# Kernel optimization log

Measured on AMD Instinct MI355X. Metric: run time of the kernel, lower is better.

## Reference

```python
import jax, jax.numpy as jnp
import numpy as np

N, E, D, H = 20000, 320000, 128, 256
NUM_FINE = 2


def _mlp(x, W1, b1, W2, b2):
    # Linear -> relu -> Linear -> relu (dropout rate 0.0 is identity)
    h = jax.nn.relu(x @ W1 + b1)
    return jax.nn.relu(h @ W2 + b2)


def setup_inputs() -> dict:
    key = jax.random.key(0)
    ks = jax.random.split(key, 12)

    def p(k, shape):
        fan_in = shape[0]
        return jax.random.normal(k, shape, jnp.float32) * (1.0 / fan_in) ** 0.5

    return {
        "nodes": jax.random.normal(ks[0], (N, D), jnp.float32),
        "edges": jax.random.normal(ks[1], (E, D), jnp.float32),
        "senders": jax.random.randint(ks[2], (E,), 0, N, jnp.int32),
        "receivers": jax.random.randint(ks[3], (E,), 0, N, jnp.int32),
        # embed node MLP: D -> H -> D
        "Wn1": p(ks[4], (D, H)), "bn1": jnp.zeros((H,), jnp.float32),
        "Wn2": p(ks[5], (H, D)), "bn2": jnp.zeros((D,), jnp.float32),
        # embed edge MLP: D -> H -> D
        "We1": p(ks[6], (D, H)), "be1": jnp.zeros((H,), jnp.float32),
        "We2": p(ks[7], (H, D)), "be2": jnp.zeros((D,), jnp.float32),
        # edge model MLP: 3D -> H -> D  (concat[src, dest, edge_attr])
        "Wed1": p(ks[8], (3 * D, H)), "bed1": jnp.zeros((H,), jnp.float32),
        "Wed2": p(ks[9], (H, D)), "bed2": jnp.zeros((D,), jnp.float32),
        # node model MLP: 2D -> H -> D  (concat[x, segment_sum(edge_attr)])
        "Wnd1": p(ks[10], (2 * D, H)), "bnd1": jnp.zeros((H,), jnp.float32),
        "Wnd2": p(ks[11], (H, D)), "bnd2": jnp.zeros((D,), jnp.float32),
    }


def reference(nodes, edges, senders, receivers,
              Wn1, bn1, Wn2, bn2, We1, be1, We2, be2,
              Wed1, bed1, Wed2, bed2, Wnd1, bnd1, Wnd2, bnd2):
    # Embed stage (EmbedMetaLayer)
    x = _mlp(nodes, Wn1, bn1, Wn2, bn2)   # (N, D)
    e = _mlp(edges, We1, be1, We2, be2)   # (E, D)

    pooled = []
    for _ in range(NUM_FINE):
        # EdgeModel: gather src/dest node feats, concat with edge feats, MLP
        edge_in = jnp.concatenate([x[senders], x[receivers], e], axis=-1)  # (E, 3D)
        e = _mlp(edge_in, Wed1, bed1, Wed2, bed2)                           # (E, D)
        # NodeModel: scatter-add edge feats to receiver nodes, concat, MLP
        agg = jax.ops.segment_sum(e, receivers, num_segments=N)            # (N, D)
        x = _mlp(jnp.concatenate([x, agg], axis=-1), Wnd1, bnd1, Wnd2, bnd2)  # (N, D)
        # global_add_pooling: vmap(jnp.sum) over nodes -> per-node feature sum (N,)
        pooled.append(jnp.sum(x, axis=-1))
    # concatenate along last axis of the 1-D pooled vectors -> (NUM_FINE * N,)
    return jnp.concatenate(pooled, axis=-1)
```

## Files before the change

kernel.cpp:

```cpp
#include <hip/hip_runtime.h>
#include <stdint.h>

#define N_NODES 20000
#define N_EDGES 320000

typedef __attribute__((ext_vector_type(8)))  __bf16        bf16x8;
typedef __attribute__((ext_vector_type(16))) float         f32x16;
typedef __attribute__((ext_vector_type(4)))  float         f32x4v;
typedef __attribute__((ext_vector_type(4)))  uint32_t      u32x4;
typedef __attribute__((ext_vector_type(8)))  unsigned short us8;
typedef __attribute__((ext_vector_type(2)))  unsigned short us2;

static __device__ __forceinline__ unsigned short cvt_bf16(float f) {
  uint32_t u = __builtin_bit_cast(uint32_t, f);
  u = (u + 0x7fffu + ((u >> 16) & 1u)) >> 16;
  return (unsigned short)u;
}
static __device__ __forceinline__ float cvt_f32(unsigned short h) {
  uint32_t u = ((uint32_t)h) << 16;
  return __builtin_bit_cast(float, u);
}

static __device__ __forceinline__ void gll16(const void* g, void* l) {
  __builtin_amdgcn_global_load_lds(
      (const __attribute__((address_space(1))) unsigned int*)g,
      (__attribute__((address_space(3))) unsigned int*)l, 16, 0, 0);
}

#define WAITV(n) do { \
  if ((n) == 0)      asm volatile("s_waitcnt vmcnt(0)" ::: "memory"); \
  else if ((n) == 2) asm volatile("s_waitcnt vmcnt(2)" ::: "memory"); \
  else if ((n) == 4) asm volatile("s_waitcnt vmcnt(4)" ::: "memory"); \
  else if ((n) == 6) asm volatile("s_waitcnt vmcnt(6)" ::: "memory"); \
  else               asm volatile("s_waitcnt vmcnt(8)" ::: "memory"); \
} while (0)

__global__ void pack_w(const float* __restrict__ W, unsigned short* __restrict__ out,
                       int K, int Ncols) {
  int idx = blockIdx.x * 256 + threadIdx.x;
  int total = K * Ncols;
  if (idx >= total) return;
  int e    = idx & 7;
  int lane = (idx >> 3) & 63;
  int t    = idx >> 9;
  int ntiles = Ncols >> 5;
  int nt = t % ntiles;
  int ks = t / ntiles;
  int k = ks * 16 + (lane >> 5) * 8 + e;
  int c = nt * 32 + (lane & 31);
  out[idx] = cvt_bf16(W[(size_t)k * Ncols + c]);
}

__global__ void pack_w2(const float* __restrict__ W, unsigned short* __restrict__ out) {
  int idx = blockIdx.x * 256 + threadIdx.x;
  if (idx >= 32768) return;
  int e    = idx & 7;
  int lane = (idx >> 3) & 63;
  int t    = idx >> 9;
  int nt = t & 3, ks = t >> 2;
  int k = ks * 16 + ((lane >> 5) << 2) + (e & 3) + ((e >> 2) << 3);
  int c = nt * 32 + (lane & 31);
  out[idx] = cvt_bf16(W[(size_t)k * 128 + c]);
}

__global__ void hist_k(const int* __restrict__ recv, int* __restrict__ cnt, int n) {
  int i = blockIdx.x * 256 + threadIdx.x;
  if (i < n) atomicAdd(&cnt[recv[i]], 1);
}

__global__ void scan_k(const int* __restrict__ cnt, int* __restrict__ off,
                       int* __restrict__ cursor, int n) {
  __shared__ int part[1024];
  int t = threadIdx.x;
  int chunk = (n + 1023) / 1024;
  int base = t * chunk;
  int s = 0;
  for (int i = 0; i < chunk; ++i) { int idx = base + i; if (idx < n) s += cnt[idx]; }
  part[t] = s;
  __syncthreads();
  for (int d = 1; d < 1024; d <<= 1) {
    int v = (t >= d) ? part[t - d] : 0;
    __syncthreads();
    part[t] += v;
    __syncthreads();
  }
  int prefix = (t > 0) ? part[t - 1] : 0;
  for (int i = 0; i < chunk; ++i) {
    int idx = base + i;
    if (idx < n) { off[idx] = prefix; cursor[idx] = prefix; prefix += cnt[idx]; }
  }
  if (t == 1023) off[n] = part[1023];
}

__global__ void fill_k(const int* __restrict__ recv, int* __restrict__ cursor,
                       int* __restrict__ eid, int n) {
  int i = blockIdx.x * 256 + threadIdx.x;
  if (i < n) {
    int p = atomicAdd(&cursor[recv[i]], 1);
    eid[p] = i;
  }
}

__global__ void agg_k(const unsigned short* __restrict__ eb, const int* __restrict__ off,
                      const int* __restrict__ eid, unsigned short* __restrict__ aggb, int n) {
  int node = blockIdx.x * 4 + (threadIdx.x >> 6);
  if (node >= n) return;
  int lane = threadIdx.x & 63;
  float a0 = 0.f, a1 = 0.f;
  int s = off[node], t = off[node + 1];
  for (int q = s; q < t; ++q) {
    int ei = eid[q];
    us2 v = *(const us2*)(eb + (size_t)ei * 128 + lane * 2);
    a0 += cvt_f32(v[0]);
    a1 += cvt_f32(v[1]);
  }
  us2 r; r[0] = cvt_bf16(a0); r[1] = cvt_bf16(a1);
  *(us2*)(aggb + (size_t)node * 128 + lane * 2) = r;
}

template <int KIN, int MODE, int POOL>
__global__ __launch_bounds__(256, 2)
void mlp_kernel(const float* __restrict__ srcf,
                const unsigned short* __restrict__ xb,
                const unsigned short* __restrict__ ebuf,
                const unsigned short* __restrict__ aggb,
                const int* __restrict__ senders,
                const int* __restrict__ receivers,
                const unsigned short* __restrict__ P1,
                const float* __restrict__ b1,
                const unsigned short* __restrict__ P2,
                const float* __restrict__ b2,
                unsigned short* __restrict__ dst,
                float* __restrict__ pool_out,
                int nrows) {
  constexpr int NS1 = KIN / 32;
  constexpr int ROWOPS = (MODE == 0) ? 4 : 2;
  __shared__ __align__(16) unsigned char lds[49152];

  const int tid  = threadIdx.x;
  const int lane = tid & 63;
  const int wid  = tid >> 6;
  const int g    = lane >> 5;
  const int l31  = lane & 31;
  const int rowBlock = blockIdx.x << 7;

  const unsigned char* P1b = (const unsigned char*)P1;
  const unsigned char* P2b = (const unsigned char*)P2;

  int grow = rowBlock + wid * 32 + l31;
  if (grow >= nrows) grow = nrows - 1;

  const unsigned short *pS = nullptr, *pR = nullptr, *pE = nullptr;
  const unsigned short *pX = nullptr, *pAg = nullptr;
  const float* fb = nullptr;
  if constexpr (MODE == 0) {
    fb = srcf + (size_t)grow * KIN;
  } else if constexpr (MODE == 1) {
    pS = xb + (size_t)senders[grow] * 128;
    pR = xb + (size_t)receivers[grow] * 128;
    pE = ebuf + (size_t)grow * 128;
  } else {
    pX  = xb + (size_t)grow * 128;
    pAg = aggb + (size_t)grow * 128;
  }

  auto STG1 = [&](int s) {
    unsigned char* bW = lds + (s % 3) * 16384;
#pragma unroll
    for (int c = 0; c < 4; ++c)
      gll16(P1b + (size_t)s * 16384 + c * 4096 + tid * 16,
            bW + c * 4096 + wid * 1024);
  };
  auto STG2 = [&](int c) {
    unsigned char* bW = lds + ((c + NS1) % 3) * 16384;
#pragma unroll
    for (int q = 0; q < 4; ++q)
      gll16(P2b + (size_t)c * 16384 + q * 4096 + tid * 16,
            bW + q * 4096 + wid * 1024);
  };

  auto LROW = [&](int s, us8* o) {
    const int k0s = s * 32;
    const unsigned short* p;
    if constexpr (MODE == 1) {
      const int seg = k0s >> 7;
      p = (seg == 0) ? pS : (seg == 1) ? pR : pE;
    } else {
      p = (k0s >> 7) ? pAg : pX;
    }
    const int ko = k0s & 127;
    o[0] = *(const us8*)(p + ko + g * 8);
    o[1] = *(const us8*)(p + ko + 16 + g * 8);
  };
  auto LROWF = [&](int s, f32x4v* rf) {
    const float* p = fb + s * 32 + g * 8;
    rf[0] = *(const f32x4v*)(p);
    rf[1] = *(const f32x4v*)(p + 4);
    rf[2] = *(const f32x4v*)(p + 16);
    rf[3] = *(const f32x4v*)(p + 20);
  };
  auto MKBR = [&](const f32x4v* rf, bf16x8& b0v, bf16x8& b1v) {
    us8 h0, h1;
#pragma unroll
    for (int e = 0; e < 4; ++e) {
      h0[e] = cvt_bf16(rf[0][e]); h0[4 + e] = cvt_bf16(rf[1][e]);
      h1[e] = cvt_bf16(rf[2][e]); h1[4 + e] = cvt_bf16(rf[3][e]);
    }
    b0v = __builtin_bit_cast(bf16x8, h0);
    b1v = __builtin_bit_cast(bf16x8, h1);
  };

  f32x16 acc1[8];
#pragma unroll
  for (int t = 0; t < 8; ++t)
#pragma unroll
    for (int k = 0; k < 16; ++k) acc1[t][k] = 0.0f;

  auto COMPUTE = [&](const unsigned char* bW, bf16x8 b0v, bf16x8 b1v) {
    __builtin_amdgcn_s_setprio(1);
#pragma unroll
    for (int kc = 0; kc < 2; ++kc) {
      const bf16x8 bv = kc ? b1v : b0v;
#pragma unroll
      for (int nt = 0; nt < 8; ++nt) {
        bf16x8 av = __builtin_bit_cast(bf16x8,
            *(const us8*)(bW + (kc * 8 + nt) * 1024 + lane * 16));
        acc1[nt] = __builtin_amdgcn_mfma_f32_32x32x16_bf16(av, bv, acc1[nt], 0, 0, 0);
      }
    }
    __builtin_amdgcn_s_setprio(0);
  };

  us8    rr[4][2];
  f32x4v rf[4][4];

  STG1(0);
  if constexpr (MODE == 0) { LROWF(0, rf[0]); LROWF(1, rf[1]); LROWF(2, rf[2]); }
  else                     { LROW(0, rr[0]);  LROW(1, rr[1]);  LROW(2, rr[2]); }

#pragma unroll
  for (int s = 0; s < NS1; ++s) {
    const int w = (s == 0) ? ROWOPS * 2 : ((s + 2 < NS1) ? ROWOPS : 0);
    WAITV(w);
    asm volatile("s_waitcnt lgkmcnt(0)" ::: "memory");
    asm volatile("s_barrier" ::: "memory");
    if (s + 1 < NS1) STG1(s + 1);
    if (s + 3 < NS1) {
      if constexpr (MODE == 0) LROWF(s + 3, rf[(s + 3) & 3]);
      else                     LROW(s + 3, rr[(s + 3) & 3]);
    }
    bf16x8 b0v, b1v;
    if constexpr (MODE == 0) MKBR(rf[s & 3], b0v, b1v);
    else { b0v = __builtin_bit_cast(bf16x8, rr[s & 3][0]);
           b1v = __builtin_bit_cast(bf16x8, rr[s & 3][1]); }
    COMPUTE(lds + (s % 3) * 16384, b0v, b1v);
  }

  STG2(0);
  STG2(1);

  u32x4 pa4[16];
#pragma unroll
  for (int t = 0; t < 8; ++t) {
#pragma unroll
    for (int q4 = 0; q4 < 4; ++q4) {
      const f32x4v bv4 = *(const f32x4v*)(b1 + t * 32 + q4 * 8 + g * 4);
      float v0 = fmaxf(acc1[t][q4 * 4 + 0] + bv4[0], 0.0f);
      float v1 = fmaxf(acc1[t][q4 * 4 + 1] + bv4[1], 0.0f);
      float v2 = fmaxf(acc1[t][q4 * 4 + 2] + bv4[2], 0.0f);
      float v3 = fmaxf(acc1[t][q4 * 4 + 3] + bv4[3], 0.0f);
      uint32_t lo, hi;
      asm("v_cvt_pk_bf16_f32 %0, %1, %2" : "=v"(lo) : "v"(v0), "v"(v1));
      asm("v_cvt_pk_bf16_f32 %0, %1, %2" : "=v"(hi) : "v"(v2), "v"(v3));
      pa4[t * 2 + (q4 >> 1)][(q4 & 1) * 2 + 0] = lo;
      pa4[t * 2 + (q4 >> 1)][(q4 & 1) * 2 + 1] = hi;
    }
  }

  f32x16 acc2[4];
#pragma unroll
  for (int nt = 0; nt < 4; ++nt)
#pragma unroll
    for (int k = 0; k < 16; ++k) acc2[nt][k] = 0.0f;

#pragma unroll
  for (int c = 0; c < 4; ++c) {
    WAITV(c < 3 ? 4 : 0);
    asm volatile("s_waitcnt lgkmcnt(0)" ::: "memory");
    asm volatile("s_barrier" ::: "memory");
    if (c + 2 < 4) STG2(c + 2);
    const unsigned char* bW = lds + ((c + NS1) % 3) * 16384;
    __builtin_amdgcn_s_setprio(1);
#pragma unroll
    for (int kk = 0; kk < 4; ++kk) {
      const bf16x8 a2 = __builtin_bit_cast(bf16x8, pa4[c * 4 + kk]);
#pragma unroll
      for (int nt = 0; nt < 4; ++nt) {
        const bf16x8 bw = __builtin_bit_cast(bf16x8,
            *(const us8*)(bW + (kk * 4 + nt) * 1024 + lane * 16));
        acc2[nt] = __builtin_amdgcn_mfma_f32_32x32x16_bf16(a2, bw, acc2[nt], 0, 0, 0);
      }
    }
    __builtin_amdgcn_s_setprio(0);
  }

  float bias2[4];
#pragma unroll
  for (int nt = 0; nt < 4; ++nt) bias2[nt] = b2[nt * 32 + l31];

#pragma unroll
  for (int reg = 0; reg < 16; ++reg) {
    const int rowpat = (reg & 3) + ((reg >> 2) << 3) + g * 4;
    const int row = rowBlock + wid * 32 + rowpat;
    float vs = 0.0f;
#pragma unroll
    for (int nt = 0; nt < 4; ++nt) {
      float v = fmaxf(acc2[nt][reg] + bias2[nt], 0.0f);
      vs += v;
      if (row < nrows) dst[(size_t)row * 128 + nt * 32 + l31] = cvt_bf16(v);
    }
    if constexpr (POOL) {
#pragma unroll
      for (int m = 1; m <= 16; m <<= 1) vs += __shfl_xor(vs, m, 64);
      if (l31 == 0 && row < nrows) pool_out[row] = vs;
    }
  }
}

static constexpr size_t OFF_X    = 0;
static constexpr size_t OFF_E    = 5120000;
static constexpr size_t OFF_AGG  = 87040000;
static constexpr size_t OFF_PN1  = 92160000;
static constexpr size_t OFF_PN2  = OFF_PN1 + 65536;
static constexpr size_t OFF_PE1  = OFF_PN2 + 65536;
static constexpr size_t OFF_PE2  = OFF_PE1 + 65536;
static constexpr size_t OFF_PD1  = OFF_PE2 + 65536;
static constexpr size_t OFF_PD2  = OFF_PD1 + 196608;
static constexpr size_t OFF_PM1  = OFF_PD2 + 65536;
static constexpr size_t OFF_PM2  = OFF_PM1 + 131072;
static constexpr size_t OFF_CNT  = OFF_PM2 + 65536;
static constexpr size_t OFF_OFFS = OFF_CNT + 80000;
static constexpr size_t OFF_CUR  = OFF_OFFS + 80004;
static constexpr size_t OFF_EID  = OFF_CUR + 80000;

extern "C" void kernel_launch(void* const* d_in, const int* in_sizes, int n_in,
                              void* d_out, int out_size, void* d_ws, size_t ws_size,
                              hipStream_t stream) {
  const float* nodes = (const float*)d_in[0];
  const float* edges = (const float*)d_in[1];
  const int* senders = (const int*)d_in[2];
  const int* receivers = (const int*)d_in[3];
  const float* Wn1 = (const float*)d_in[4];  const float* bn1 = (const float*)d_in[5];
  const float* Wn2 = (const float*)d_in[6];  const float* bn2 = (const float*)d_in[7];
  const float* We1 = (const float*)d_in[8];  const float* be1 = (const float*)d_in[9];
  const float* We2 = (const float*)d_in[10]; const float* be2 = (const float*)d_in[11];
  const float* Wed1 = (const float*)d_in[12]; const float* bed1 = (const float*)d_in[13];
  const float* Wed2 = (const float*)d_in[14]; const float* bed2 = (const float*)d_in[15];
  const float* Wnd1 = (const float*)d_in[16]; const float* bnd1 = (const float*)d_in[17];
  const float* Wnd2 = (const float*)d_in[18]; const float* bnd2 = (const float*)d_in[19];

  char* ws = (char*)d_ws;
  unsigned short* xb   = (unsigned short*)(ws + OFF_X);
  unsigned short* eb   = (unsigned short*)(ws + OFF_E);
  unsigned short* aggb = (unsigned short*)(ws + OFF_AGG);
  unsigned short* Pn1  = (unsigned short*)(ws + OFF_PN1);
  unsigned short* Pn2  = (unsigned short*)(ws + OFF_PN2);
  unsigned short* Pe1  = (unsigned short*)(ws + OFF_PE1);
  unsigned short* Pe2  = (unsigned short*)(ws + OFF_PE2);
  unsigned short* Pd1  = (unsigned short*)(ws + OFF_PD1);
  unsigned short* Pd2  = (unsigned short*)(ws + OFF_PD2);
  unsigned short* Pm1  = (unsigned short*)(ws + OFF_PM1);
  unsigned short* Pm2  = (unsigned short*)(ws + OFF_PM2);
  int* cnt    = (int*)(ws + OFF_CNT);
  int* offs   = (int*)(ws + OFF_OFFS);
  int* cursor = (int*)(ws + OFF_CUR);
  int* eid    = (int*)(ws + OFF_EID);
  float* outp = (float*)d_out;

  pack_w<<<128, 256, 0, stream>>>(Wn1, Pn1, 128, 256);
  pack_w2<<<128, 256, 0, stream>>>(Wn2, Pn2);
  pack_w<<<128, 256, 0, stream>>>(We1, Pe1, 128, 256);
  pack_w2<<<128, 256, 0, stream>>>(We2, Pe2);
  pack_w<<<384, 256, 0, stream>>>(Wed1, Pd1, 384, 256);
  pack_w2<<<128, 256, 0, stream>>>(Wed2, Pd2);
  pack_w<<<256, 256, 0, stream>>>(Wnd1, Pm1, 256, 256);
  pack_w2<<<128, 256, 0, stream>>>(Wnd2, Pm2);

  hipMemsetAsync(cnt, 0, (size_t)N_NODES * 4, stream);
  hist_k<<<1250, 256, 0, stream>>>(receivers, cnt, N_EDGES);
  scan_k<<<1, 1024, 0, stream>>>(cnt, offs, cursor, N_NODES);
  fill_k<<<1250, 256, 0, stream>>>(receivers, cursor, eid, N_EDGES);

  const int nodeBlocks = (N_NODES + 127) / 128;
  const int edgeBlocks = N_EDGES / 128;

  mlp_kernel<128, 0, 0><<<nodeBlocks, 256, 0, stream>>>(
      nodes, nullptr, nullptr, nullptr, nullptr, nullptr,
      Pn1, bn1, Pn2, bn2, xb, nullptr, N_NODES);
  mlp_kernel<128, 0, 0><<<edgeBlocks, 256, 0, stream>>>(
      edges, nullptr, nullptr, nullptr, nullptr, nullptr,
      Pe1, be1, Pe2, be2, eb, nullptr, N_EDGES);

  for (int it = 0; it < 2; ++it) {
    mlp_kernel<384, 1, 0><<<edgeBlocks, 256, 0, stream>>>(
        nullptr, xb, eb, nullptr, senders, receivers,
        Pd1, bed1, Pd2, bed2, eb, nullptr, N_EDGES);
    agg_k<<<(N_NODES + 3) / 4, 256, 0, stream>>>(eb, offs, eid, aggb, N_NODES);
    mlp_kernel<256, 2, 1><<<nodeBlocks, 256, 0, stream>>>(
        nullptr, xb, nullptr, aggb, nullptr, nullptr,
        Pm1, bnd1, Pm2, bnd2, xb, outp + (size_t)it * N_NODES, N_NODES);
  }
}
```

Measured before the change: 514.2 us.

## Process two K-stages per barrier with 4-slot LDS weight ring

Restructures the MLP kernel's K-loop to handle two 32-wide K stages per barrier, using a 4-slot (64KB) LDS ring for the weight tiles instead of a 3-slot 48KB ring. Row prefetch depth grows to four stages, and the second GEMM also does two chunks per barrier. The aim is to halve barrier and waitcnt synchronisation points and give more MFMA work between syncs. In exchange, the larger LDS footprint and extra prefetch registers may reduce occupancy below the 2 blocks per CU requested by launch bounds, and the second GEMM now waits for all outstanding loads (vmcnt 0) at each barrier.

```diff
diff --git a/kernel.cpp b/kernel.cpp
--- a/kernel.cpp
+++ b/kernel.cpp
@@ -29,10 +29,9 @@
 
 #define WAITV(n) do { \
   if ((n) == 0)      asm volatile("s_waitcnt vmcnt(0)" ::: "memory"); \
-  else if ((n) == 2) asm volatile("s_waitcnt vmcnt(2)" ::: "memory"); \
   else if ((n) == 4) asm volatile("s_waitcnt vmcnt(4)" ::: "memory"); \
-  else if ((n) == 6) asm volatile("s_waitcnt vmcnt(6)" ::: "memory"); \
-  else               asm volatile("s_waitcnt vmcnt(8)" ::: "memory"); \
+  else if ((n) == 8) asm volatile("s_waitcnt vmcnt(8)" ::: "memory"); \
+  else               asm volatile("s_waitcnt vmcnt(12)" ::: "memory"); \
 } while (0)
 
 __global__ void pack_w(const float* __restrict__ W, unsigned short* __restrict__ out,
@@ -134,8 +133,8 @@
                 float* __restrict__ pool_out,
                 int nrows) {
   constexpr int NS1 = KIN / 32;
-  constexpr int ROWOPS = (MODE == 0) ? 4 : 2;
-  __shared__ __align__(16) unsigned char lds[49152];
+  constexpr int NP  = NS1 / 2;
+  __shared__ __align__(16) unsigned char lds[65536];
 
   const int tid  = threadIdx.x;
   const int lane = tid & 63;
@@ -165,14 +164,14 @@
   }
 
   auto STG1 = [&](int s) {
-    unsigned char* bW = lds + (s % 3) * 16384;
+    unsigned char* bW = lds + (s & 3) * 16384;
 #pragma unroll
     for (int c = 0; c < 4; ++c)
       gll16(P1b + (size_t)s * 16384 + c * 4096 + tid * 16,
             bW + c * 4096 + wid * 1024);
   };
   auto STG2 = [&](int c) {
-    unsigned char* bW = lds + ((c + NS1) % 3) * 16384;
+    unsigned char* bW = lds + ((c + NS1) & 3) * 16384;
 #pragma unroll
     for (int q = 0; q < 4; ++q)
       gll16(P2b + (size_t)c * 16384 + q * 4096 + tid * 16,
@@ -217,7 +216,6 @@
     for (int k = 0; k < 16; ++k) acc1[t][k] = 0.0f;
 
   auto COMPUTE = [&](const unsigned char* bW, bf16x8 b0v, bf16x8 b1v) {
-    __builtin_amdgcn_s_setprio(1);
 #pragma unroll
     for (int kc = 0; kc < 2; ++kc) {
       const bf16x8 bv = kc ? b1v : b0v;
@@ -228,32 +226,42 @@
         acc1[nt] = __builtin_amdgcn_mfma_f32_32x32x16_bf16(av, bv, acc1[nt], 0, 0, 0);
       }
     }
-    __builtin_amdgcn_s_setprio(0);
   };
 
   us8    rr[4][2];
   f32x4v rf[4][4];
 
-  STG1(0);
-  if constexpr (MODE == 0) { LROWF(0, rf[0]); LROWF(1, rf[1]); LROWF(2, rf[2]); }
-  else                     { LROW(0, rr[0]);  LROW(1, rr[1]);  LROW(2, rr[2]); }
-
-#pragma unroll
-  for (int s = 0; s < NS1; ++s) {
-    const int w = (s == 0) ? ROWOPS * 2 : ((s + 2 < NS1) ? ROWOPS : 0);
+  STG1(0); STG1(1);
+  if constexpr (MODE == 0) { LROWF(0, rf[0]); LROWF(1, rf[1]); LROWF(2, rf[2]); LROWF(3, rf[3]); }
+  else                     { LROW(0, rr[0]);  LROW(1, rr[1]);  LROW(2, rr[2]);  LROW(3, rr[3]); }
+
+#pragma unroll
+  for (int p = 0; p < NP; ++p) {
+    const int s0 = 2 * p, s1 = 2 * p + 1;
+    const int w = (p + 1 < NP) ? ((MODE == 0) ? 8 : 4) : 0;
     WAITV(w);
     asm volatile("s_waitcnt lgkmcnt(0)" ::: "memory");
     asm volatile("s_barrier" ::: "memory");
-    if (s + 1 < NS1) STG1(s + 1);
-    if (s + 3 < NS1) {
-      if constexpr (MODE == 0) LROWF(s + 3, rf[(s + 3) & 3]);
-      else                     LROW(s + 3, rr[(s + 3) & 3]);
-    }
-    bf16x8 b0v, b1v;
-    if constexpr (MODE == 0) MKBR(rf[s & 3], b0v, b1v);
-    else { b0v = __builtin_bit_cast(bf16x8, rr[s & 3][0]);
-           b1v = __builtin_bit_cast(bf16x8, rr[s & 3][1]); }
-    COMPUTE(lds + (s % 3) * 16384, b0v, b1v);
+
+    bf16x8 a0v, a1v, c0v, c1v;
+    if constexpr (MODE == 0) { MKBR(rf[s0 & 3], a0v, a1v); MKBR(rf[s1 & 3], c0v, c1v); }
+    else {
+      a0v = __builtin_bit_cast(bf16x8, rr[s0 & 3][0]); a1v = __builtin_bit_cast(bf16x8, rr[s0 & 3][1]);
+      c0v = __builtin_bit_cast(bf16x8, rr[s1 & 3][0]); c1v = __builtin_bit_cast(bf16x8, rr[s1 & 3][1]);
+    }
+
+    if (p + 1 < NP) {
+      STG1(s0 + 2); STG1(s1 + 2);
+      if (p + 2 < NP) {
+        if constexpr (MODE == 0) { LROWF(s0 + 4, rf[(s0 + 4) & 3]); LROWF(s1 + 4, rf[(s1 + 4) & 3]); }
+        else                     { LROW(s0 + 4, rr[(s0 + 4) & 3]);  LROW(s1 + 4, rr[(s1 + 4) & 3]); }
+      }
+    }
+
+    __builtin_amdgcn_s_setprio(1);
+    COMPUTE(lds + (s0 & 3) * 16384, a0v, a1v);
+    COMPUTE(lds + (s1 & 3) * 16384, c0v, c1v);
+    __builtin_amdgcn_s_setprio(0);
   }
 
   STG2(0);
@@ -284,21 +292,25 @@
     for (int k = 0; k < 16; ++k) acc2[nt][k] = 0.0f;
 
 #pragma unroll
-  for (int c = 0; c < 4; ++c) {
-    WAITV(c < 3 ? 4 : 0);
+  for (int q = 0; q < 2; ++q) {
+    WAITV(0);
     asm volatile("s_waitcnt lgkmcnt(0)" ::: "memory");
     asm volatile("s_barrier" ::: "memory");
-    if (c + 2 < 4) STG2(c + 2);
-    const unsigned char* bW = lds + ((c + NS1) % 3) * 16384;
+    if (q == 0) { STG2(2); STG2(3); }
     __builtin_amdgcn_s_setprio(1);
 #pragma unroll
-    for (int kk = 0; kk < 4; ++kk) {
-      const bf16x8 a2 = __builtin_bit_cast(bf16x8, pa4[c * 4 + kk]);
-#pragma unroll
-      for (int nt = 0; nt < 4; ++nt) {
-        const bf16x8 bw = __builtin_bit_cast(bf16x8,
-            *(const us8*)(bW + (kk * 4 + nt) * 1024 + lane * 16));
-        acc2[nt] = __builtin_amdgcn_mfma_f32_32x32x16_bf16(a2, bw, acc2[nt], 0, 0, 0);
+    for (int ci = 0; ci < 2; ++ci) {
+      const int c = q * 2 + ci;
+      const unsigned char* bW = lds + ((c + NS1) & 3) * 16384;
+#pragma unroll
+      for (int kk = 0; kk < 4; ++kk) {
+        const bf16x8 a2 = __builtin_bit_cast(bf16x8, pa4[c * 4 + kk]);
+#pragma unroll
+        for (int nt = 0; nt < 4; ++nt) {
+          const bf16x8 bw = __builtin_bit_cast(bf16x8,
+              *(const us8*)(bW + (kk * 4 + nt) * 1024 + lane * 16));
+          acc2[nt] = __builtin_amdgcn_mfma_f32_32x32x16_bf16(a2, bw, acc2[nt], 0, 0, 0);
+        }
       }
     }
     __builtin_amdgcn_s_setprio(0);
```

Result: no change. 521.3 us (+1.4%).
